# Kernel optimization log

Hardware: AMD Instinct MI355X
Metric: run time of the kernel (lower is better)

The kernel has to match this reference:

```python
import jax, jax.numpy as jnp
import numpy as np

B, N, T1, T2, K = 16, 2048, 12, 64, 3


def setup_inputs() -> dict:
    key = jax.random.key(0)
    ks = jax.random.split(key, 16)
    g = lambda k, s, sc=1.0: jax.random.normal(k, s, dtype=jnp.float32) * sc
    X = g(ks[0], (B, N, 1, T1))
    A = jax.random.uniform(ks[1], (N, N), dtype=jnp.float32)
    Vs = g(ks[2], (N, N), 1.0 / np.sqrt(N))
    bs = g(ks[3], (N, N), 0.01)
    W1 = jax.random.uniform(ks[4], (T1,), dtype=jnp.float32)
    W2 = g(ks[5], (1, T1), 1.0)
    W3 = jax.random.uniform(ks[6], (1,), dtype=jnp.float32)
    Ve = g(ks[7], (T1, T1), 1.0 / np.sqrt(T1))
    be = g(ks[8], (T1, T1), 0.01)
    U1 = jax.random.uniform(ks[9], (N,), dtype=jnp.float32) / np.sqrt(N)
    U2 = g(ks[10], (1, N), 1.0 / np.sqrt(N))
    U3 = jax.random.uniform(ks[11], (1,), dtype=jnp.float32)
    Wcheb = g(ks[12], (K, T1, T2), 1.0 / np.sqrt(T1))
    bcheb = jnp.zeros((T2,), jnp.float32)
    return dict(X=X, A=A, Vs=Vs, bs=bs, W1=W1, W2=W2, W3=W3, Ve=Ve, be=be,
                U1=U1, U2=U2, U3=U3, Wcheb=Wcheb, bcheb=bcheb)


def reference(X, A, Vs, bs, W1, W2, W3, Ve, be, U1, U2, U3, Wcheb, bcheb):
    # ---- SpatialAtt (C=1). NOTE: faithful to source, the resulting A_hat = A*S
    # is computed in the torch forward but NEVER used downstream (gcn params are
    # built from plain A). jit will DCE this branch.
    W1x = jnp.einsum('bnct,t->bnc', X, W1)            # [B,N,1]
    W3x = jnp.einsum('c,bnct->bnt', W3, X)            # [B,N,T1]
    Ssc = jnp.einsum('bnt,bmt->bnm', jnp.einsum('bnc,ct->bnt', W1x, W2), W3x) + bs
    S = jax.nn.softmax(jnp.einsum('nm,bml->bnl', Vs, jax.nn.softmax(Ssc, axis=1)), axis=1)
    _A_hat = A[None] * S  # unused (matches source)

    # ---- TemporalAtt
    xT = jnp.transpose(X, (0, 3, 2, 1))               # [B,T1,1,N]
    E1 = jnp.einsum('btc,cn->btn', jnp.einsum('btcn,n->btc', xT, U1), U2)  # [B,T1,N]
    U3x = jnp.einsum('c,bnct->bnt', U3, X)            # [B,N,T1]
    Esc = jnp.einsum('btn,bns->bts', E1, U3x) + be    # [B,T1,T1]
    E = jax.nn.softmax(jnp.einsum('ts,bsu->btu', Ve, jax.nn.softmax(Esc, axis=1)), axis=1)

    # E.repeat(1,N,1).view(B,N,T,T) broadcasts the same [T,T] per node
    x2 = X[:, :, 0, :]                                # [B,N,T1]
    X_hat = jnp.einsum('bnt,btu->bnu', x2, E)         # [B,N,T1]

    # ---- ChebConv, sym normalization, lambda_max = 2 -> L_hat = -D^{-1/2} A D^{-1/2}
    # deg from row-sums (scatter over edge_index[0]); aggregation at target (col),
    # so applying L_hat is a transpose-matmul in dense form.
    deg = A.sum(axis=1)
    dis = jnp.where(deg > 0, jax.lax.rsqrt(jnp.where(deg > 0, deg, 1.0)), 0.0)
    M = -(dis[:, None] * A * dis[None, :])            # [N,N]
    Lx = lambda h: jnp.einsum('rc,brt->bct', M, h)    # out[col] += norm * x[row]

    Tx_prev = X_hat
    out = jnp.einsum('bnt,to->bno', X_hat, Wcheb[0])
    Tx = Lx(X_hat)
    if K > 1:
        out = out + jnp.einsum('bnt,to->bno', Tx, Wcheb[1])
    for k in range(2, K):
        Tx_new = 2.0 * Lx(Tx) - Tx_prev
        out = out + jnp.einsum('bnt,to->bno', Tx_new, Wcheb[k])
        Tx_prev, Tx = Tx, Tx_new
    out = jax.nn.relu(out + bcheb)
    return out.reshape(B, N, 1, T2)
```

## Files before the change

### kernel.cpp

```cpp
#include <hip/hip_runtime.h>
#include <math.h>

#define NN 2048
#define BB 16
#define T1D 12
#define T2D 64
#define JJ 192

typedef short short8 __attribute__((ext_vector_type(8)));
typedef float f32x4 __attribute__((ext_vector_type(4)));

#define OFF_DIS   0
#define OFF_E     2048
#define OFF_XH    4608
#define OFF_P1    (OFF_XH + NN*JJ)
#define OFF_P2    (OFF_P1 + NN*JJ)
#define OFF_XHBT  (OFF_P2 + NN*JJ)
#define OFF_P1BT  (OFF_XHBT + NN*JJ/2)
#define OFF_ABT   (OFF_P1BT + NN*JJ/2)

__device__ inline ushort f2bf(float f) {
    union { float f; unsigned int u; } x; x.f = f;
    unsigned int u = x.u + 0x7fffu + ((x.u >> 16) & 1u);
    return (ushort)(u >> 16);
}

__global__ __launch_bounds__(256) void k_degE(const float* __restrict__ A,
                                              const float* __restrict__ X,
                                              const float* __restrict__ U1,
                                              const float* __restrict__ U2,
                                              const float* __restrict__ U3,
                                              const float* __restrict__ be,
                                              const float* __restrict__ Ve,
                                              float* __restrict__ dis,
                                              float* __restrict__ E_ws) {
    __shared__ float red[24][256];
    __shared__ float es[T1D][T1D];
    int tid = threadIdx.x;

    if (blockIdx.x < 512) {
        int wid = tid >> 6, lane = tid & 63;
        int r = blockIdx.x * 4 + wid;
        const float4* Ar = (const float4*)(A + (size_t)r * NN);
        float s = 0.f;
#pragma unroll
        for (int i = 0; i < 8; ++i) {
            float4 v = Ar[i * 64 + lane];
            s += v.x + v.y + v.z + v.w;
        }
#pragma unroll
        for (int off = 32; off > 0; off >>= 1) s += __shfl_down(s, off);
        if (lane == 0) dis[r] = (s > 0.f) ? rsqrtf(s) : 0.f;
        return;
    }

    int b = blockIdx.x - 512;
    float accr[T1D], accc[T1D];
#pragma unroll
    for (int t = 0; t < T1D; ++t) { accr[t] = 0.f; accc[t] = 0.f; }
    for (int n = tid; n < NN; n += 256) {
        const float* xp = X + ((size_t)b * NN + n) * T1D;
        float x[T1D];
        *(float4*)&x[0] = *(const float4*)&xp[0];
        *(float4*)&x[4] = *(const float4*)&xp[4];
        *(float4*)&x[8] = *(const float4*)&xp[8];
        float u1 = U1[n], u2 = U2[n];
#pragma unroll
        for (int t = 0; t < T1D; ++t) {
            accr[t] += x[t] * u1;
            accc[t] += x[t] * u2;
        }
    }
#pragma unroll
    for (int t = 0; t < T1D; ++t) {
        red[t][tid] = accr[t];
        red[12 + t][tid] = accc[t];
    }
    __syncthreads();
    for (int s = 128; s > 0; s >>= 1) {
        if (tid < s) {
#pragma unroll
            for (int a = 0; a < 24; ++a) red[a][tid] += red[a][tid + s];
        }
        __syncthreads();
    }
    float u3 = U3[0];
    if (tid < T1D) {
        int s = tid;
        float cs = red[12 + s][0] * u3;
        float vals[T1D];
        float m = -1e30f;
#pragma unroll
        for (int t = 0; t < T1D; ++t) {
            vals[t] = red[t][0] * cs + be[t * T1D + s];
            m = fmaxf(m, vals[t]);
        }
        float sum = 0.f;
#pragma unroll
        for (int t = 0; t < T1D; ++t) { vals[t] = expf(vals[t] - m); sum += vals[t]; }
        float inv = 1.f / sum;
#pragma unroll
        for (int t = 0; t < T1D; ++t) es[t][s] = vals[t] * inv;
    }
    __syncthreads();
    if (tid < T1D) {
        int u = tid;
        float vals[T1D];
        float m = -1e30f;
#pragma unroll
        for (int t = 0; t < T1D; ++t) {
            float acc = 0.f;
#pragma unroll
            for (int s = 0; s < T1D; ++s) acc += Ve[t * T1D + s] * es[s][u];
            vals[t] = acc;
            m = fmaxf(m, acc);
        }
        float sum = 0.f;
#pragma unroll
        for (int t = 0; t < T1D; ++t) { vals[t] = expf(vals[t] - m); sum += vals[t]; }
        float inv = 1.f / sum;
#pragma unroll
        for (int t = 0; t < T1D; ++t) E_ws[b * 144 + t * T1D + u] = vals[t] * inv;
    }
}

__global__ __launch_bounds__(256) void k_mid(const float* __restrict__ A,
                                             const float* __restrict__ dis,
                                             const float* __restrict__ X,
                                             const float* __restrict__ E_ws,
                                             ushort* __restrict__ AbT,
                                             float* __restrict__ Xh,
                                             ushort* __restrict__ Xhbt) {
    __shared__ float lds[5504];
    int t = threadIdx.x;

    if (blockIdx.x < 1024) {
        int c0 = (blockIdx.x & 31) * 64, k0 = (blockIdx.x >> 5) * 64;
#pragma unroll
        for (int i = 0; i < 4; ++i) {
            int idx = t + i * 256;
            int kr = idx >> 4, c4 = idx & 15;
            float4 v = *(const float4*)&A[(size_t)(k0 + kr) * NN + c0 + c4 * 4];
            float dk = dis[k0 + kr];
            lds[(c4 * 4 + 0) * 65 + kr] = v.x * dk;
            lds[(c4 * 4 + 1) * 65 + kr] = v.y * dk;
            lds[(c4 * 4 + 2) * 65 + kr] = v.z * dk;
            lds[(c4 * 4 + 3) * 65 + kr] = v.w * dk;
        }
        __syncthreads();
        int cl = t >> 2, ck = (t & 3) * 16;
        float dc = dis[c0 + cl];
        union { ushort us[8]; uint4 v; } p0, p1;
#pragma unroll
        for (int e = 0; e < 8; ++e) p0.us[e] = f2bf(lds[cl * 65 + ck + e] * dc);
#pragma unroll
        for (int e = 0; e < 8; ++e) p1.us[e] = f2bf(lds[cl * 65 + ck + 8 + e] * dc);
        *(uint4*)&AbT[(size_t)(c0 + cl) * NN + k0 + ck] = p0.v;
        *(uint4*)&AbT[(size_t)(c0 + cl) * NN + k0 + ck + 8] = p1.v;
        return;
    }

    int n0 = (blockIdx.x - 1024) * 16;
    float* EL = lds + 3200;
#pragma unroll
    for (int i = 0; i < 9; ++i) {
        int idx = t + i * 256;
        if (idx < 2304) EL[idx] = E_ws[idx];
    }
    __syncthreads();
    {
        int nr = t >> 4, b = t & 15;
        const float* xp = X + ((size_t)b * NN + n0 + nr) * T1D;
        float x[T1D];
        *(float4*)&x[0] = *(const float4*)&xp[0];
        *(float4*)&x[4] = *(const float4*)&xp[4];
        *(float4*)&x[8] = *(const float4*)&xp[8];
        const float* Eb = EL + b * 144;
#pragma unroll
        for (int u = 0; u < T1D; ++u) {
            float acc = 0.f;
#pragma unroll
            for (int tt = 0; tt < T1D; ++tt) acc += x[tt] * Eb[tt * T1D + u];
            lds[nr * 200 + b * T1D + u] = acc;
        }
    }
    __syncthreads();
#pragma unroll
    for (int i = 0; i < 3; ++i) {
        int idx4 = t + i * 256;
        int row = idx4 / 48, c4 = idx4 % 48;
        *(float4*)&Xh[(size_t)(n0 + row) * JJ + c4 * 4] =
            *(float4*)&lds[row * 200 + c4 * 4];
    }
    if (t < JJ) {
        union { ushort us[8]; uint4 v; } p0, p1;
#pragma unroll
        for (int nr = 0; nr < 8; ++nr) p0.us[nr] = f2bf(lds[nr * 200 + t]);
#pragma unroll
        for (int nr = 0; nr < 8; ++nr) p1.us[nr] = f2bf(lds[(8 + nr) * 200 + t]);
        *(uint4*)&Xhbt[(size_t)t * NN + n0] = p0.v;
        *(uint4*)&Xhbt[(size_t)t * NN + n0 + 8] = p1.v;
    }
}

template<int NFRAG, bool WBT>
__global__ __launch_bounds__(512) void k_gemm(const ushort* __restrict__ AbT,
                                              const ushort* __restrict__ Zbt,
                                              float* __restrict__ P,
                                              ushort* __restrict__ Pbt) {
    __shared__ float lds[8 * NFRAG * 64 * 4];
    int tid = threadIdx.x;
    int wave = tid >> 6, lane = tid & 63;
    int jl = lane & 15;
    int kl = (lane >> 4) * 8;
    int c0 = blockIdx.x * 16;
    int j0 = blockIdx.y * (16 * NFRAG);
    int kbase = wave * 256 + kl;

    const ushort* arow = AbT + (size_t)(c0 + jl) * NN + kbase;
    f32x4 acc[NFRAG];
#pragma unroll
    for (int n = 0; n < NFRAG; ++n) acc[n] = (f32x4)0.f;

#pragma unroll
    for (int ch = 0; ch < 8; ++ch) {
        int koff = ch * 32;
        short8 a = *(const short8*)&arow[koff];
        short8 bfr[NFRAG];
#pragma unroll
        for (int n = 0; n < NFRAG; ++n)
            bfr[n] = *(const short8*)&Zbt[(size_t)(j0 + n * 16 + jl) * NN + kbase + koff];
#pragma unroll
        for (int n = 0; n < NFRAG; ++n)
            acc[n] = __builtin_amdgcn_mfma_f32_16x16x32_bf16(a, bfr[n], acc[n], 0, 0, 0);
    }

#pragma unroll
    for (int n = 0; n < NFRAG; ++n)
        *(f32x4*)&lds[((wave * NFRAG + n) * 64 + lane) * 4] = acc[n];
    __syncthreads();

    const int NOUT = 16 * 16 * NFRAG;
    for (int o = tid; o < NOUT; o += 512) {
        int c_idx = o / (16 * NFRAG);
        int j_idx = o % (16 * NFRAG);
        int n = j_idx >> 4, col = j_idx & 15;
        int lidx = ((c_idx >> 2) * 16 + col) * 4 + (c_idx & 3);
        float s = 0.f;
#pragma unroll
        for (int w = 0; w < 8; ++w) s += lds[(w * NFRAG + n) * 256 + lidx];
        P[(size_t)(c0 + c_idx) * JJ + j0 + j_idx] = s;
        if (WBT) Pbt[(size_t)(j0 + j_idx) * NN + c0 + c_idx] = f2bf(s);
    }
}

__global__ __launch_bounds__(256) void k_out(const float* __restrict__ Xh,
                                             const float* __restrict__ P1,
                                             const float* __restrict__ P2,
                                             const float* __restrict__ Wcheb,
                                             const float* __restrict__ bcheb,
                                             float* __restrict__ out) {
    int g = blockIdx.x * 256 + threadIdx.x;
    int o = g & 63;
    int row = g >> 6;
    int b = row >> 11;
    int n = row & 2047;
    int base = n * JJ + b * T1D;
    const float* xh = Xh + base;
    const float* p1 = P1 + base;
    const float* p2 = P2 + base;
    const float* W0 = Wcheb;
    const float* W1 = Wcheb + 768;
    const float* W2 = Wcheb + 1536;
    float acc = bcheb[o];
#pragma unroll
    for (int t = 0; t < T1D; ++t) {
        float w0 = W0[t * 64 + o], w1 = W1[t * 64 + o], w2 = W2[t * 64 + o];
        acc += xh[t] * (w0 - w2) - p1[t] * w1 + 2.f * p2[t] * w2;
    }
    out[g] = fmaxf(acc, 0.f);
}

extern "C" void kernel_launch(void* const* d_in, const int* in_sizes, int n_in,
                              void* d_out, int out_size, void* d_ws, size_t ws_size,
                              hipStream_t stream) {
    const float* X  = (const float*)d_in[0];
    const float* A  = (const float*)d_in[1];
    const float* Ve = (const float*)d_in[7];
    const float* be = (const float*)d_in[8];
    const float* U1 = (const float*)d_in[9];
    const float* U2 = (const float*)d_in[10];
    const float* U3 = (const float*)d_in[11];
    const float* Wc = (const float*)d_in[12];
    const float* bc = (const float*)d_in[13];
    float* out = (float*)d_out;

    float* w     = (float*)d_ws;
    float* dis   = w + OFF_DIS;
    float* E     = w + OFF_E;
    float* Xh    = w + OFF_XH;
    float* P1    = w + OFF_P1;
    float* P2    = w + OFF_P2;
    ushort* Xhbt = (ushort*)(w + OFF_XHBT);
    ushort* P1bt = (ushort*)(w + OFF_P1BT);
    ushort* AbT  = (ushort*)(w + OFF_ABT);

    k_degE<<<528, 256, 0, stream>>>(A, X, U1, U2, U3, be, Ve, dis, E);
    k_mid<<<1152, 256, 0, stream>>>(A, dis, X, E, AbT, Xh, Xhbt);
    k_gemm<3, true ><<<dim3(128, 4), 512, 0, stream>>>(AbT, Xhbt, P1, P1bt);
    k_gemm<3, false><<<dim3(128, 4), 512, 0, stream>>>(AbT, P1bt, P2, nullptr);
    k_out<<<(BB * NN * T2D) / 256, 256, 0, stream>>>(Xh, P1, P2, Wc, bc, out);
}
```

Baseline: 180.6 us.

## Split GEMM over K with atomic accumulation and separate bf16 transpose kernel

The GEMM drops the 4-way split over the output columns (3 fragments per block). Instead each block computes all 12 fragments for one 256-wide slice of the reduction dimension, 8 slices in all. Partial sums are combined with float atomicAdd into zeroed P buffers, and a new small kernel then builds the transposed bf16 copy of P1. The aim is to reuse each A fragment across all 192 output columns rather than reloading it per column group. The cost is more registers per thread, global atomics, an extra memset and an extra kernel launch, and a summation order that is no longer deterministic.

```diff
diff --git a/kernel.cpp b/kernel.cpp
--- a/kernel.cpp
+++ b/kernel.cpp
@@ -203,54 +203,74 @@
     }
 }
 
-template<int NFRAG, bool WBT>
-__global__ __launch_bounds__(512) void k_gemm(const ushort* __restrict__ AbT,
+__global__ __launch_bounds__(256) void k_gemm(const ushort* __restrict__ AbT,
                                               const ushort* __restrict__ Zbt,
-                                              float* __restrict__ P,
-                                              ushort* __restrict__ Pbt) {
-    __shared__ float lds[8 * NFRAG * 64 * 4];
+                                              float* __restrict__ P) {
+    __shared__ float lds[4 * 12 * 256];
     int tid = threadIdx.x;
     int wave = tid >> 6, lane = tid & 63;
     int jl = lane & 15;
     int kl = (lane >> 4) * 8;
     int c0 = blockIdx.x * 16;
-    int j0 = blockIdx.y * (16 * NFRAG);
-    int kbase = wave * 256 + kl;
+    int kbase = blockIdx.y * 256 + wave * 64 + kl;
 
     const ushort* arow = AbT + (size_t)(c0 + jl) * NN + kbase;
-    f32x4 acc[NFRAG];
-#pragma unroll
-    for (int n = 0; n < NFRAG; ++n) acc[n] = (f32x4)0.f;
-
-#pragma unroll
-    for (int ch = 0; ch < 8; ++ch) {
+    f32x4 acc[12];
+#pragma unroll
+    for (int n = 0; n < 12; ++n) acc[n] = (f32x4)0.f;
+
+    for (int ch = 0; ch < 2; ++ch) {
         int koff = ch * 32;
         short8 a = *(const short8*)&arow[koff];
-        short8 bfr[NFRAG];
-#pragma unroll
-        for (int n = 0; n < NFRAG; ++n)
-            bfr[n] = *(const short8*)&Zbt[(size_t)(j0 + n * 16 + jl) * NN + kbase + koff];
-#pragma unroll
-        for (int n = 0; n < NFRAG; ++n)
+        short8 bfr[12];
+#pragma unroll
+        for (int n = 0; n < 12; ++n)
+            bfr[n] = *(const short8*)&Zbt[(size_t)(n * 16 + jl) * NN + kbase + koff];
+#pragma unroll
+        for (int n = 0; n < 12; ++n)
             acc[n] = __builtin_amdgcn_mfma_f32_16x16x32_bf16(a, bfr[n], acc[n], 0, 0, 0);
     }
 
 #pragma unroll
-    for (int n = 0; n < NFRAG; ++n)
-        *(f32x4*)&lds[((wave * NFRAG + n) * 64 + lane) * 4] = acc[n];
-    __syncthreads();
-
-    const int NOUT = 16 * 16 * NFRAG;
-    for (int o = tid; o < NOUT; o += 512) {
-        int c_idx = o / (16 * NFRAG);
-        int j_idx = o % (16 * NFRAG);
+    for (int n = 0; n < 12; ++n)
+        *(f32x4*)&lds[((wave * 12 + n) << 8) + (lane << 2)] = acc[n];
+    __syncthreads();
+
+    for (int o = tid; o < 3072; o += 256) {
+        int c_idx = o / JJ;
+        int j_idx = o - c_idx * JJ;
         int n = j_idx >> 4, col = j_idx & 15;
         int lidx = ((c_idx >> 2) * 16 + col) * 4 + (c_idx & 3);
-        float s = 0.f;
-#pragma unroll
-        for (int w = 0; w < 8; ++w) s += lds[(w * NFRAG + n) * 256 + lidx];
-        P[(size_t)(c0 + c_idx) * JJ + j0 + j_idx] = s;
-        if (WBT) Pbt[(size_t)(j0 + j_idx) * NN + c0 + c_idx] = f2bf(s);
+        float s = lds[(0 * 12 + n) * 256 + lidx] + lds[(1 * 12 + n) * 256 + lidx]
+                + lds[(2 * 12 + n) * 256 + lidx] + lds[(3 * 12 + n) * 256 + lidx];
+        atomicAdd(&P[(size_t)(c0 + c_idx) * JJ + j_idx], s);
+    }
+}
+
+__global__ __launch_bounds__(256) void k_t(const float* __restrict__ P,
+                                           ushort* __restrict__ Pbt) {
+    __shared__ float lds[16][193];
+    int t = threadIdx.x;
+    int c0 = blockIdx.x * 16;
+#pragma unroll
+    for (int i = 0; i < 3; ++i) {
+        int idx = t + i * 256;
+        int row = idx / 48, c4 = idx % 48;
+        float4 v = *(const float4*)&P[(size_t)(c0 + row) * JJ + c4 * 4];
+        lds[row][c4 * 4 + 0] = v.x;
+        lds[row][c4 * 4 + 1] = v.y;
+        lds[row][c4 * 4 + 2] = v.z;
+        lds[row][c4 * 4 + 3] = v.w;
+    }
+    __syncthreads();
+    if (t < JJ) {
+        union { ushort us[8]; uint4 v; } p0, p1;
+#pragma unroll
+        for (int n = 0; n < 8; ++n) p0.us[n] = f2bf(lds[n][t]);
+#pragma unroll
+        for (int n = 0; n < 8; ++n) p1.us[n] = f2bf(lds[8 + n][t]);
+        *(uint4*)&Pbt[(size_t)t * NN + c0] = p0.v;
+        *(uint4*)&Pbt[(size_t)t * NN + c0 + 8] = p1.v;
     }
 }
 
@@ -305,9 +325,12 @@
     ushort* P1bt = (ushort*)(w + OFF_P1BT);
     ushort* AbT  = (ushort*)(w + OFF_ABT);
 
+    hipMemsetAsync(P1, 0, (size_t)2 * NN * JJ * sizeof(float), stream);
+
     k_degE<<<528, 256, 0, stream>>>(A, X, U1, U2, U3, be, Ve, dis, E);
     k_mid<<<1152, 256, 0, stream>>>(A, dis, X, E, AbT, Xh, Xhbt);
-    k_gemm<3, true ><<<dim3(128, 4), 512, 0, stream>>>(AbT, Xhbt, P1, P1bt);
-    k_gemm<3, false><<<dim3(128, 4), 512, 0, stream>>>(AbT, P1bt, P2, nullptr);
+    k_gemm<<<dim3(128, 8), 256, 0, stream>>>(AbT, Xhbt, P1);
+    k_t<<<128, 256, 0, stream>>>(P1, P1bt);
+    k_gemm<<<dim3(128, 8), 256, 0, stream>>>(AbT, P1bt, P2);
     k_out<<<(BB * NN * T2D) / 256, 256, 0, stream>>>(Xh, P1, P2, Wc, bc, out);
 }
```

Result: slower. 196.7 us (+8.9%).

## Fuse Chebyshev output projection into second GEMM epilogue and coalesce bf16 transpose writes

Applied to the files above, without the earlier changes.

The final output kernel is merged into the epilogue of the second GEMM. The reduced P2 tile stays in shared memory and is combined with Xh, P1 and the Chebyshev weights to write the ReLU output directly, so the P2 buffer and one kernel launch go away. The first GEMM now writes its bf16 transposed copy as 16-byte vector stores staged through LDS instead of scattered 2-byte stores. In exchange, each block's epilogue does more work and uses more registers, which may hurt occupancy.

```diff
diff --git a/kernel.cpp b/kernel.cpp
--- a/kernel.cpp
+++ b/kernel.cpp
@@ -14,8 +14,7 @@
 #define OFF_E     2048
 #define OFF_XH    4608
 #define OFF_P1    (OFF_XH + NN*JJ)
-#define OFF_P2    (OFF_P1 + NN*JJ)
-#define OFF_XHBT  (OFF_P2 + NN*JJ)
+#define OFF_XHBT  (OFF_P1 + NN*JJ)
 #define OFF_P1BT  (OFF_XHBT + NN*JJ/2)
 #define OFF_ABT   (OFF_P1BT + NN*JJ/2)
 
@@ -203,82 +202,102 @@
     }
 }
 
-template<int NFRAG, bool WBT>
+template<int MODE>
 __global__ __launch_bounds__(512) void k_gemm(const ushort* __restrict__ AbT,
                                               const ushort* __restrict__ Zbt,
                                               float* __restrict__ P,
-                                              ushort* __restrict__ Pbt) {
-    __shared__ float lds[8 * NFRAG * 64 * 4];
+                                              ushort* __restrict__ Pbt,
+                                              const float* __restrict__ P1,
+                                              const float* __restrict__ Xh,
+                                              const float* __restrict__ Wcheb,
+                                              const float* __restrict__ bcheb,
+                                              float* __restrict__ out) {
+    __shared__ float lds[8 * 3 * 256 + 16 * 48];
+    float* Pred = lds + 6144;
     int tid = threadIdx.x;
     int wave = tid >> 6, lane = tid & 63;
     int jl = lane & 15;
     int kl = (lane >> 4) * 8;
     int c0 = blockIdx.x * 16;
-    int j0 = blockIdx.y * (16 * NFRAG);
+    int j0 = blockIdx.y * 48;
     int kbase = wave * 256 + kl;
 
     const ushort* arow = AbT + (size_t)(c0 + jl) * NN + kbase;
-    f32x4 acc[NFRAG];
-#pragma unroll
-    for (int n = 0; n < NFRAG; ++n) acc[n] = (f32x4)0.f;
+    f32x4 acc[3];
+#pragma unroll
+    for (int n = 0; n < 3; ++n) acc[n] = (f32x4)0.f;
 
 #pragma unroll
     for (int ch = 0; ch < 8; ++ch) {
         int koff = ch * 32;
         short8 a = *(const short8*)&arow[koff];
-        short8 bfr[NFRAG];
-#pragma unroll
-        for (int n = 0; n < NFRAG; ++n)
+        short8 bfr[3];
+#pragma unroll
+        for (int n = 0; n < 3; ++n)
             bfr[n] = *(const short8*)&Zbt[(size_t)(j0 + n * 16 + jl) * NN + kbase + koff];
 #pragma unroll
-        for (int n = 0; n < NFRAG; ++n)
+        for (int n = 0; n < 3; ++n)
             acc[n] = __builtin_amdgcn_mfma_f32_16x16x32_bf16(a, bfr[n], acc[n], 0, 0, 0);
     }
 
 #pragma unroll
-    for (int n = 0; n < NFRAG; ++n)
-        *(f32x4*)&lds[((wave * NFRAG + n) * 64 + lane) * 4] = acc[n];
-    __syncthreads();
-
-    const int NOUT = 16 * 16 * NFRAG;
-    for (int o = tid; o < NOUT; o += 512) {
-        int c_idx = o / (16 * NFRAG);
-        int j_idx = o % (16 * NFRAG);
+    for (int n = 0; n < 3; ++n)
+        *(f32x4*)&lds[((wave * 3 + n) << 8) + (lane << 2)] = acc[n];
+    __syncthreads();
+
+    for (int o = tid; o < 768; o += 512) {
+        int c_idx = o / 48;
+        int j_idx = o - c_idx * 48;
         int n = j_idx >> 4, col = j_idx & 15;
         int lidx = ((c_idx >> 2) * 16 + col) * 4 + (c_idx & 3);
         float s = 0.f;
 #pragma unroll
-        for (int w = 0; w < 8; ++w) s += lds[(w * NFRAG + n) * 256 + lidx];
-        P[(size_t)(c0 + c_idx) * JJ + j0 + j_idx] = s;
-        if (WBT) Pbt[(size_t)(j0 + j_idx) * NN + c0 + c_idx] = f2bf(s);
-    }
-}
-
-__global__ __launch_bounds__(256) void k_out(const float* __restrict__ Xh,
-                                             const float* __restrict__ P1,
-                                             const float* __restrict__ P2,
-                                             const float* __restrict__ Wcheb,
-                                             const float* __restrict__ bcheb,
-                                             float* __restrict__ out) {
-    int g = blockIdx.x * 256 + threadIdx.x;
-    int o = g & 63;
-    int row = g >> 6;
-    int b = row >> 11;
-    int n = row & 2047;
-    int base = n * JJ + b * T1D;
-    const float* xh = Xh + base;
-    const float* p1 = P1 + base;
-    const float* p2 = P2 + base;
-    const float* W0 = Wcheb;
-    const float* W1 = Wcheb + 768;
-    const float* W2 = Wcheb + 1536;
-    float acc = bcheb[o];
-#pragma unroll
-    for (int t = 0; t < T1D; ++t) {
-        float w0 = W0[t * 64 + o], w1 = W1[t * 64 + o], w2 = W2[t * 64 + o];
-        acc += xh[t] * (w0 - w2) - p1[t] * w1 + 2.f * p2[t] * w2;
-    }
-    out[g] = fmaxf(acc, 0.f);
+        for (int w = 0; w < 8; ++w) s += lds[(w * 3 + n) * 256 + lidx];
+        Pred[c_idx * 48 + j_idx] = s;
+        if (MODE == 0) P[(size_t)(c0 + c_idx) * JJ + j0 + j_idx] = s;
+    }
+    __syncthreads();
+
+    if (MODE == 0) {
+        if (tid < 48) {
+            union { ushort us[8]; uint4 v; } q0, q1;
+#pragma unroll
+            for (int e = 0; e < 8; ++e) q0.us[e] = f2bf(Pred[e * 48 + tid]);
+#pragma unroll
+            for (int e = 0; e < 8; ++e) q1.us[e] = f2bf(Pred[(8 + e) * 48 + tid]);
+            *(uint4*)&Pbt[(size_t)(j0 + tid) * NN + c0] = q0.v;
+            *(uint4*)&Pbt[(size_t)(j0 + tid) * NN + c0 + 8] = q1.v;
+        }
+    } else {
+        int o = tid & 63, pair = tid >> 6;
+        const float* W0 = Wcheb;
+        const float* W1 = Wcheb + 768;
+        const float* W2 = Wcheb + 1536;
+        float w0m2[T1D], w1a[T1D], w2a[T1D];
+#pragma unroll
+        for (int t = 0; t < T1D; ++t) {
+            float w2v = W2[t * 64 + o];
+            w0m2[t] = W0[t * 64 + o] - w2v;
+            w1a[t] = W1[t * 64 + o];
+            w2a[t] = 2.f * w2v;
+        }
+        float bco = bcheb[o];
+#pragma unroll
+        for (int it = 0; it < 8; ++it) {
+            int pi = pair + it * 8;
+            int ni = pi >> 2, bi = pi & 3;
+            int n = c0 + ni;
+            int b = blockIdx.y * 4 + bi;
+            const float* xh = Xh + (size_t)n * JJ + b * T1D;
+            const float* p1 = P1 + (size_t)n * JJ + b * T1D;
+            const float* p2 = Pred + ni * 48 + bi * T1D;
+            float a = bco;
+#pragma unroll
+            for (int t = 0; t < T1D; ++t)
+                a += xh[t] * w0m2[t] - p1[t] * w1a[t] + p2[t] * w2a[t];
+            out[(size_t)((b << 11) + n) * 64 + o] = fmaxf(a, 0.f);
+        }
+    }
 }
 
 extern "C" void kernel_launch(void* const* d_in, const int* in_sizes, int n_in,
@@ -300,14 +319,14 @@
     float* E     = w + OFF_E;
     float* Xh    = w + OFF_XH;
     float* P1    = w + OFF_P1;
-    float* P2    = w + OFF_P2;
     ushort* Xhbt = (ushort*)(w + OFF_XHBT);
     ushort* P1bt = (ushort*)(w + OFF_P1BT);
     ushort* AbT  = (ushort*)(w + OFF_ABT);
 
     k_degE<<<528, 256, 0, stream>>>(A, X, U1, U2, U3, be, Ve, dis, E);
     k_mid<<<1152, 256, 0, stream>>>(A, dis, X, E, AbT, Xh, Xhbt);
-    k_gemm<3, true ><<<dim3(128, 4), 512, 0, stream>>>(AbT, Xhbt, P1, P1bt);
-    k_gemm<3, false><<<dim3(128, 4), 512, 0, stream>>>(AbT, P1bt, P2, nullptr);
-    k_out<<<(BB * NN * T2D) / 256, 256, 0, stream>>>(Xh, P1, P2, Wc, bc, out);
-}
+    k_gemm<0><<<dim3(128, 4), 512, 0, stream>>>(AbT, Xhbt, P1, P1bt,
+                                                nullptr, nullptr, nullptr, nullptr, nullptr);
+    k_gemm<1><<<dim3(128, 4), 512, 0, stream>>>(AbT, P1bt, nullptr, nullptr,
+                                                P1, Xh, Wc, bc, out);
+}
```

New measurement: 168.9 us. -6.4%, faster.
